# Kernel optimization log

Hardware: AMD Instinct MI355X
Metric: run time of the kernel (lower is better)

Reference implementation:

```python
import jax, jax.numpy as jnp
import numpy as np

B, T, D, H, L, OUT = 16, 48, 256, 8, 3, 6
STYLE, SKILL = 64, 64


def _ln(x, g, b):
    m = jnp.mean(x, -1, keepdims=True)
    v = jnp.mean((x - m) ** 2, -1, keepdims=True)
    return (x - m) * jax.lax.rsqrt(v + 1e-5) * g + b


def _gelu(x):
    return jax.nn.gelu(x, approximate=False)  # torch 'gelu' activation is exact erf form


def _mha(q_in, kv_in, qkv_w, qkv_b, o_w, o_b, mask):
    d = q_in.shape[-1]
    hd = d // H
    wq, wk, wv = jnp.split(qkv_w, 3, 0)
    bq, bk, bv = jnp.split(qkv_b, 3, 0)

    def heads(x, w, b):
        y = x @ w.T + b
        return y.reshape(y.shape[0], y.shape[1], H, hd)

    q, k, v = heads(q_in, wq, bq), heads(kv_in, wk, bk), heads(kv_in, wv, bv)
    s = jnp.einsum('bqhd,bkhd->bhqk', q, k) / np.float32(np.sqrt(hd))
    if mask is not None:
        s = jnp.where(mask, jnp.float32(-1e9), s)
    a = jax.nn.softmax(s, -1)
    o = jnp.einsum('bhqk,bkhd->bqhd', a, v).reshape(q_in.shape[0], q_in.shape[1], d)
    return o @ o_w.T + o_b


def _pos_encoding():
    pos = jnp.arange(T, dtype=jnp.float32)[:, None]
    div = jnp.exp(jnp.arange(0, D, 2, dtype=jnp.float32) * (-np.log(10000.0) / D))
    pe = jnp.zeros((T, D), jnp.float32)
    pe = pe.at[:, 0::2].set(jnp.sin(pos * div))
    pe = pe.at[:, 1::2].set(jnp.cos(pos * div))
    return pe


def setup_inputs() -> dict:
    key = jax.random.key(0)
    ks = iter(jax.random.split(key, 40))

    def rn(shape, s=0.05):
        return jax.random.normal(next(ks), shape, jnp.float32) * s

    return {
        'z_style': jax.random.normal(next(ks), (B, STYLE), jnp.float32),
        'z_skill': jax.random.normal(next(ks), (B, SKILL), jnp.float32),
        'start_token': jnp.zeros((1, 1, OUT), jnp.float32),
        'mem_w1': rn((D, STYLE + SKILL)), 'mem_b1': jnp.zeros((D,), jnp.float32),
        'mem_ln_g': jnp.ones((D,), jnp.float32), 'mem_ln_b': jnp.zeros((D,), jnp.float32),
        'mem_w2': rn((D, D)), 'mem_b2': jnp.zeros((D,), jnp.float32),
        'emb_w': rn((D, OUT)), 'emb_b': jnp.zeros((D,), jnp.float32),
        'sa_qkv_w': rn((L, 3 * D, D)), 'sa_qkv_b': jnp.zeros((L, 3 * D), jnp.float32),
        'sa_o_w': rn((L, D, D)), 'sa_o_b': jnp.zeros((L, D), jnp.float32),
        'ca_qkv_w': rn((L, 3 * D, D)), 'ca_qkv_b': jnp.zeros((L, 3 * D), jnp.float32),
        'ca_o_w': rn((L, D, D)), 'ca_o_b': jnp.zeros((L, D), jnp.float32),
        'ln1_g': jnp.ones((L, D), jnp.float32), 'ln1_b': jnp.zeros((L, D), jnp.float32),
        'ln2_g': jnp.ones((L, D), jnp.float32), 'ln2_b': jnp.zeros((L, D), jnp.float32),
        'ln3_g': jnp.ones((L, D), jnp.float32), 'ln3_b': jnp.zeros((L, D), jnp.float32),
        'ff1_w': rn((L, 4 * D, D)), 'ff1_b': jnp.zeros((L, 4 * D), jnp.float32),
        'ff2_w': rn((L, D, 4 * D)), 'ff2_b': jnp.zeros((L, D), jnp.float32),
        'op_w1': rn((D // 2, D)), 'op_b1': jnp.zeros((D // 2,), jnp.float32),
        'op_w2': rn((OUT, D // 2)), 'op_b2': jnp.zeros((OUT,), jnp.float32),
    }


def reference(z_style, z_skill, start_token, mem_w1, mem_b1, mem_ln_g, mem_ln_b,
              mem_w2, mem_b2, emb_w, emb_b, sa_qkv_w, sa_qkv_b, sa_o_w, sa_o_b,
              ca_qkv_w, ca_qkv_b, ca_o_w, ca_o_b, ln1_g, ln1_b, ln2_g, ln2_b,
              ln3_g, ln3_b, ff1_w, ff1_b, ff2_w, ff2_b, op_w1, op_b1, op_w2, op_b2):
    # memory: [B,1,D] expanded to seq_len (identical rows, as in the torch module)
    cond = jnp.concatenate([z_style, z_skill], -1)
    h = _gelu(_ln(cond @ mem_w1.T + mem_b1, mem_ln_g, mem_ln_b))
    memory = jnp.broadcast_to((h @ mem_w2.T + mem_b2)[:, None, :], (B, T, D))

    pe = _pos_encoding()
    causal = jnp.triu(jnp.ones((T, T), bool), 1)  # True = masked (future)
    layer_ps = (sa_qkv_w, sa_qkv_b, sa_o_w, sa_o_b, ca_qkv_w, ca_qkv_b, ca_o_w,
                ca_o_b, ln1_g, ln1_b, ln2_g, ln2_b, ln3_g, ln3_b,
                ff1_w, ff1_b, ff2_w, ff2_b)

    def layer_step(x, p):
        (sqw, sqb, sow, sob, cqw, cqb, cow, cob, g1, b1, g2, b2, g3, b3,
         f1w, f1b, f2w, f2b) = p
        # post-norm TransformerDecoderLayer (torch default norm_first=False)
        x = _ln(x + _mha(x, x, sqw, sqb, sow, sob, causal), g1, b1)
        x = _ln(x + _mha(x, memory, cqw, cqb, cow, cob, None), g2, b2)
        x = _ln(x + (_gelu(x @ f1w.T + f1b) @ f2w.T + f2b), g3, b3)
        return x, None

    def t_step(inputs, t):
        # Causal mask => decoded[:, t] depends only on inputs[:, :t+1]; running the
        # padded full-length decoder reproduces the torch growing-prefix loop exactly.
        x = inputs @ emb_w.T + emb_b + pe[None]
        dec, _ = jax.lax.scan(layer_step, x, layer_ps)
        d_t = jax.lax.dynamic_slice(dec, (0, t, 0), (B, 1, D))[:, 0]
        out_t = _gelu(d_t @ op_w1.T + op_b1) @ op_w2.T + op_b2
        inputs = jax.lax.dynamic_update_slice(inputs, out_t[:, None, :], (0, t + 1, 0))
        return inputs, out_t

    inputs0 = jnp.zeros((B, T, OUT), jnp.float32).at[:, 0:1, :].set(
        jnp.broadcast_to(start_token, (B, 1, OUT)))
    _, ys = jax.lax.scan(t_step, inputs0, jnp.arange(T))
    return jnp.transpose(ys, (1, 0, 2))  # [B, T, OUT]
```

## Files before the change

kernel.cpp:

```cpp
#include <hip/hip_runtime.h>
#include <hip/hip_bf16.h>
#include <math.h>

#define NGRP 16
#define GWG  8
#define NBLK (NGRP*GWG)
#define NTHR 512
#define TSEQ 48
#define DDIM 256
#define HDIM 32
#define NLAY 3
#define NOUT 6

#define CNT_OFF   0u
#define CNT_BYTES 16384u
#define GRP_OFF   16384u
#define GRP_STRF  5120u
#define PO_F   0
#define PF_F   2048
#define CAL_F  4096
#define WB_OFF 360448u
#define WOFF_QKV 0u
#define WOFF_WO  589824u
#define WOFF_F1  786432u
#define WOFF_F2  1572864u
#define WOFF_OP1 2359296u
#define NCVT     2392064u

typedef __attribute__((address_space(1))) const unsigned int gu32;
typedef __attribute__((address_space(3))) unsigned int lu32;

__device__ __forceinline__ void gl_lds16(const unsigned short* g, unsigned short* l) {
  __builtin_amdgcn_global_load_lds((gu32*)g, (lu32*)l, 16, 0, 0);
}
__device__ __forceinline__ void bfp(unsigned int u, float& lo, float& hi) {
  union { unsigned int i; float f; } a, b;
  a.i = u << 16; b.i = u & 0xffff0000u; lo = a.f; hi = b.f;
}
__device__ __forceinline__ float gelu_exact(float x) {
  return 0.5f * x * (1.0f + erff(x * 0.70710678118654752f));
}
__device__ __forceinline__ float dot8(const uint4& u, const float* x, int k0) {
  float lo, hi, acc = 0.f;
  bfp(u.x, lo, hi); acc += x[k0  ]*lo + x[k0+1]*hi;
  bfp(u.y, lo, hi); acc += x[k0+2]*lo + x[k0+3]*hi;
  bfp(u.z, lo, hi); acc += x[k0+4]*lo + x[k0+5]*hi;
  bfp(u.w, lo, hi); acc += x[k0+6]*lo + x[k0+7]*hi;
  return acc;
}

__global__ void convert_bf16(const float* qkv, const float* ow, const float* f1,
                             const float* f2, const float* w1, unsigned char* ws) {
  __hip_bfloat16* dst = (__hip_bfloat16*)(ws + WB_OFF);
  size_t stride = (size_t)gridDim.x * blockDim.x;
  for (size_t i = (size_t)blockIdx.x * blockDim.x + threadIdx.x; i < NCVT; i += stride) {
    float v;
    if      (i < WOFF_WO)  v = qkv[i];
    else if (i < WOFF_F1)  v = ow[i - WOFF_WO];
    else if (i < WOFF_F2)  v = f1[i - WOFF_F1];
    else if (i < WOFF_OP1) v = f2[i - WOFF_F2];
    else                   v = w1[i - WOFF_OP1];
    dst[i] = __float2bfloat16(v);
  }
}

__global__ void precompute_ca(const float* zs, const float* zk,
                              const float* mw1, const float* mb1,
                              const float* mlg, const float* mlb,
                              const float* mw2, const float* mb2,
                              const float* cqw, const float* cqb,
                              const float* cow, const float* cob,
                              unsigned char* ws) {
  const int g = blockIdx.x & 15, l = blockIdx.x >> 4;
  const int tid = threadIdx.x;
  __shared__ float cond[128], h[256], mvv[256], vv[256], lred[16];

  auto lnstat = [&](float v, float& m, float& rs) {
    float a = v, b = v * v;
    #pragma unroll
    for (int off = 32; off; off >>= 1) { a += __shfl_xor(a, off); b += __shfl_xor(b, off); }
    if ((tid & 63) == 0) { lred[tid >> 6] = a; lred[4 + (tid >> 6)] = b; }
    __syncthreads();
    float sa = lred[0]+lred[1]+lred[2]+lred[3];
    float sb = lred[4]+lred[5]+lred[6]+lred[7];
    m = sa * (1.0f/256.0f);
    rs = rsqrtf(sb * (1.0f/256.0f) - m*m + 1e-5f);
    __syncthreads();
  };

  if (tid < 128) cond[tid] = (tid < 64) ? zs[g*64 + tid] : zk[g*64 + tid - 64];
  __syncthreads();
  float acc = mb1[tid];
  { const float* w = mw1 + (size_t)tid * 128;
    for (int k = 0; k < 128; k += 4) {
      float4 q = *(const float4*)(w + k);
      acc += q.x*cond[k] + q.y*cond[k+1] + q.z*cond[k+2] + q.w*cond[k+3];
    } }
  float m, rs; lnstat(acc, m, rs);
  h[tid] = gelu_exact((acc - m) * rs * mlg[tid] + mlb[tid]);
  __syncthreads();
  float a2 = mb2[tid];
  { const float* w = mw2 + (size_t)tid * 256;
    for (int k = 0; k < 256; k += 4) {
      float4 q = *(const float4*)(w + k);
      a2 += q.x*h[k] + q.y*h[k+1] + q.z*h[k+2] + q.w*h[k+3];
    } }
  mvv[tid] = a2;
  __syncthreads();
  float a3 = cqb[l*768 + 512 + tid];
  { const float* w = cqw + ((size_t)l*768 + 512 + tid) * 256;
    for (int k = 0; k < 256; k += 4) {
      float4 q = *(const float4*)(w + k);
      a3 += q.x*mvv[k] + q.y*mvv[k+1] + q.z*mvv[k+2] + q.w*mvv[k+3];
    } }
  vv[tid] = a3;
  __syncthreads();
  float a4 = cob[l*256 + tid];
  { const float* w = cow + ((size_t)l*256 + tid) * 256;
    for (int k = 0; k < 256; k += 4) {
      float4 q = *(const float4*)(w + k);
      a4 += q.x*vv[k] + q.y*vv[k+1] + q.z*vv[k+2] + q.w*vv[k+3];
    } }
  ((float*)(ws + GRP_OFF))[(size_t)g * GRP_STRF + CAL_F + l*256 + tid] = a4;
}

struct DecP {
  const float *start_token, *emb_w, *emb_b;
  const float *sa_qkv_b, *sa_o_b;
  const float *ln1_g, *ln1_b, *ln2_g, *ln2_b, *ln3_g, *ln3_b;
  const float *ff1_b, *ff2_b;
  const float *op_b1, *op_w2, *op_b2;
  float* out;
  unsigned char* ws;
};

__global__ __launch_bounds__(NTHR, 2) void decoder_persistent(DecP p) {
  const int g = blockIdx.x % NGRP;
  const int s = blockIdx.x / NGRP;
  const int tid = threadIdx.x;

  unsigned int* flg = (unsigned int*)(p.ws + CNT_OFF) + (size_t)g * 256;
  float* grp = (float*)(p.ws + GRP_OFF) + (size_t)g * GRP_STRF;
  float* Po = grp + PO_F;
  float* Pf = grp + PF_F;
  const float* CALW = grp + CAL_F;
  const unsigned short* WB = (const unsigned short*)(p.ws + WB_OFF);

  __shared__ __align__(16) unsigned short Rws[32768];
  __shared__ float xls[DDIM], x2ls[DDIM], red[NTHR], lred[16], fxl[128];
  __shared__ float qb[HDIM], ah[HDIM], sc[64];
  __shared__ float kc[NLAY*TSEQ*33], vc[NLAY*TSEQ*33];
  __shared__ float cals[768], obias[768], ff2b[768];
  __shared__ float ln1g[768], ln1b[768], ln2g[768], ln2b[768], ln3g[768], ln3b[768];
  __shared__ float qkvb[288], ff1b[384];
  __shared__ float embw[DDIM*NOUT], embb[DDIM];
  __shared__ float opb1[128], opw2[NOUT*128], opb2[8], OUTV[8];

  const int olin = tid >> 2, kk = tid & 3;
  const int oB = tid & 255, khB = tid >> 8;
  const int wv = tid >> 6, ln = tid & 63;

  auto stage_qkv = [&](int l) {
    #pragma unroll
    for (int r = 0; r < 6; ++r) {
      int c = (r*8 + wv)*64 + ln;
      int row = c >> 5, wc = (c & 31) ^ (row & 7);
      const unsigned short* gp = WB + WOFF_QKV
        + ((size_t)(l*768 + (row>>5)*256 + s*32 + (row&31)))*256 + wc*8;
      gl_lds16(gp, Rws + (size_t)(r*8 + wv)*512);
    }
  };
  auto stage_ff1 = [&](int l) {
    #pragma unroll
    for (int r = 0; r < 8; ++r) {
      int c = (r*8 + wv)*64 + ln;
      int row = c >> 5, wc = (c & 31) ^ (row & 7);
      const unsigned short* gp = WB + WOFF_F1
        + ((size_t)(l*1024 + s*128 + row))*256 + wc*8;
      gl_lds16(gp, Rws + (size_t)(r*8 + wv)*512);
    }
  };
  auto stage_ff2 = [&](int l) {
    #pragma unroll
    for (int r = 0; r < 8; ++r) {
      int c = (r*8 + wv)*64 + ln;
      int row = c >> 4, wc = (c & 15) ^ (row & 7);
      const unsigned short* gp = WB + WOFF_F2
        + ((size_t)(l*256 + row))*1024 + s*128 + wc*8;
      gl_lds16(gp, Rws + (size_t)(r*8 + wv)*512);
    }
  };

  uint4 pWO[2], pO1[8];
  auto ldWO = [&](int l) {
    const unsigned short* w = WB + WOFF_WO + ((size_t)(l*256 + oB))*256 + s*32 + khB*16;
    pWO[0] = *(const uint4*)(w);
    pWO[1] = *(const uint4*)(w + 8);
  };
  auto ldO1 = [&]() {
    const unsigned short* w = WB + WOFF_OP1 + (size_t)olin*256 + kk*64;
    #pragma unroll
    for (int i = 0; i < 8; ++i) pO1[i] = *(const uint4*)(w + i*8);
  };

  unsigned int barcount = 0;
  auto group_barrier = [&]() {
    __syncthreads();
    ++barcount;
    if (tid == 0)
      __hip_atomic_store(flg + s*32, barcount, __ATOMIC_RELEASE, __HIP_MEMORY_SCOPE_AGENT);
    if (tid < GWG) {
      while (__hip_atomic_load(flg + tid*32, __ATOMIC_RELAXED, __HIP_MEMORY_SCOPE_AGENT) < barcount) {}
    }
    if (tid == 0)
      (void)__hip_atomic_load(flg + s*32, __ATOMIC_ACQUIRE, __HIP_MEMORY_SCOPE_AGENT);
    __syncthreads();
  };

  auto lnstats = [&](float v, float& m, float& rs) {
    float a = v, b = v * v;
    #pragma unroll
    for (int off = 32; off; off >>= 1) { a += __shfl_xor(a, off); b += __shfl_xor(b, off); }
    if ((tid & 63) == 0) { lred[tid >> 6] = a; lred[8 + (tid >> 6)] = b; }
    __syncthreads();
    float sa = lred[0]+lred[1]+lred[2]+lred[3]+lred[4]+lred[5]+lred[6]+lred[7];
    float sb = lred[8]+lred[9]+lred[10]+lred[11]+lred[12]+lred[13]+lred[14]+lred[15];
    m = sa * (1.0f/256.0f);
    rs = rsqrtf(sb * (1.0f/256.0f) - m*m + 1e-5f);
    __syncthreads();
  };

  for (int i = tid; i < 768; i += NTHR) {
    cals[i]  = CALW[i];
    obias[i] = p.sa_o_b[i];
    ff2b[i]  = p.ff2_b[i];
    ln1g[i] = p.ln1_g[i]; ln1b[i] = p.ln1_b[i];
    ln2g[i] = p.ln2_g[i]; ln2b[i] = p.ln2_b[i];
    ln3g[i] = p.ln3_g[i]; ln3b[i] = p.ln3_b[i];
  }
  for (int i = tid; i < 288; i += NTHR) {
    int l = i / 96, r = i % 96, sect = (r >> 5), o = r & 31;
    qkvb[i] = p.sa_qkv_b[l*768 + sect*256 + s*32 + o];
  }
  for (int i = tid; i < 384; i += NTHR) {
    int l = i >> 7, o = i & 127;
    ff1b[i] = p.ff1_b[l*1024 + s*128 + o];
  }
  for (int i = tid; i < DDIM*NOUT; i += NTHR) embw[i] = p.emb_w[i];
  for (int i = tid; i < DDIM; i += NTHR) embb[i] = p.emb_b[i];
  for (int i = tid; i < 128; i += NTHR) opb1[i] = p.op_b1[i];
  for (int i = tid; i < NOUT*128; i += NTHR) opw2[i] = p.op_w2[i];
  if (tid < NOUT) { opb2[tid] = p.op_b2[tid]; OUTV[tid] = p.start_token[tid]; }

  const float divv = (tid < 256) ? expf(-0.035977892078031968f * (float)(2*(tid>>1))) : 0.f;

  stage_qkv(0);
  ldWO(0);
  __syncthreads();

  for (int t = 0; t < TSEQ; ++t) {
    for (int l = 0; l < NLAY; ++l) {
      if (l == 0) {
        __syncthreads();
        if (tid < 256) {
          float ang = (float)t * divv;
          float pe = (tid & 1) ? cosf(ang) : sinf(ang);
          float acc = embb[tid] + pe;
          #pragma unroll
          for (int j = 0; j < NOUT; ++j) acc += OUTV[j] * embw[tid*NOUT + j];
          xls[tid] = acc;
        }
      } else {
        float r2 = 0.f;
        if (tid < 256) {
          r2 = x2ls[tid] + ff2b[(l-1)*256 + tid];
          #pragma unroll
          for (int ss = 0; ss < GWG; ++ss) r2 += Pf[ss*256 + tid];
        }
        float m, rs; lnstats(r2, m, rs);
        if (tid < 256)
          xls[tid] = (r2 - m) * rs * ln3g[(l-1)*256 + tid] + ln3b[(l-1)*256 + tid];
      }
      __syncthreads();
      if (olin < 96) {
        float acc = 0.f;
        #pragma unroll
        for (int i = 0; i < 8; ++i) {
          int ii = (i + kk) & 7;
          int k0 = kk*64 + ii*8;
          const uint4 w = *(const uint4*)(Rws + olin*256 + (k0 ^ ((olin&7)<<3)));
          acc += dot8(w, xls, k0);
        }
        red[tid] = acc;
      }
      __syncthreads();
      stage_ff1(l);
      if (tid < 96) {
        float v = red[tid*4] + red[tid*4+1] + red[tid*4+2] + red[tid*4+3] + qkvb[l*96 + tid];
        int sect = tid >> 5, o = tid & 31;
        if (sect == 0) qb[o] = v;
        else if (sect == 1) kc[(l*TSEQ + t)*33 + o] = v;
        else vc[(l*TSEQ + t)*33 + o] = v;
      }
      __syncthreads();
      if (tid < 64) {
        float scj = -1e30f;
        if (tid <= t) {
          const float* kr = &kc[(l*TSEQ + tid)*33];
          float a = 0.f;
          #pragma unroll
          for (int d = 0; d < HDIM; ++d) a += qb[d] * kr[d];
          scj = a * 0.17677669529663687f;
        }
        float mx = scj;
        #pragma unroll
        for (int off = 32; off; off >>= 1) mx = fmaxf(mx, __shfl_xor(mx, off));
        float e = (tid <= t) ? expf(scj - mx) : 0.f;
        float su = e;
        #pragma unroll
        for (int off = 32; off; off >>= 1) su += __shfl_xor(su, off);
        sc[tid] = e / su;
      }
      __syncthreads();
      if (tid < 256) {
        int d = tid >> 3, jg = tid & 7;
        float acc = 0.f;
        for (int j = jg; j <= t; j += 8) acc += sc[j] * vc[(l*TSEQ + j)*33 + d];
        acc += __shfl_xor(acc, 1);
        acc += __shfl_xor(acc, 2);
        acc += __shfl_xor(acc, 4);
        if (jg == 0) ah[d] = acc;
      }
      __syncthreads();
      red[tid] = dot8(pWO[0], ah, khB*16) + dot8(pWO[1], ah, khB*16 + 8);
      __syncthreads();
      if (tid < 256) Po[s*256 + tid] = red[tid] + red[tid + 256];
      group_barrier();

      float r = 0.f;
      if (tid < 256) {
        r = xls[tid] + obias[l*256 + tid];
        #pragma unroll
        for (int ss = 0; ss < GWG; ++ss) r += Po[ss*256 + tid];
      }
      float m1, rs1; lnstats(r, m1, rs1);
      float z = 0.f;
      if (tid < 256)
        z = (r - m1)*rs1*ln1g[l*256 + tid] + ln1b[l*256 + tid] + cals[l*256 + tid];
      float m2, rs2; lnstats(z, m2, rs2);
      if (tid < 256) x2ls[tid] = (z - m2)*rs2*ln2g[l*256 + tid] + ln2b[l*256 + tid];
      __syncthreads();
      {
        float acc = 0.f;
        #pragma unroll
        for (int i = 0; i < 8; ++i) {
          int ii = (i + kk) & 7;
          int k0 = kk*64 + ii*8;
          const uint4 w = *(const uint4*)(Rws + olin*256 + (k0 ^ ((olin&7)<<3)));
          acc += dot8(w, x2ls, k0);
        }
        red[tid] = acc;
      }
      __syncthreads();
      stage_ff2(l);
      if (tid < 128)
        fxl[tid] = gelu_exact(red[tid*4] + red[tid*4+1] + red[tid*4+2] + red[tid*4+3]
                              + ff1b[l*128 + tid]);
      __syncthreads();
      {
        float acc = 0.f;
        #pragma unroll
        for (int j = 0; j < 8; ++j) {
          int k0 = khB*64 + j*8;
          const uint4 w = *(const uint4*)(Rws + oB*128 + (k0 ^ ((oB&7)<<3)));
          acc += dot8(w, fxl, k0);
        }
        red[tid] = acc;
      }
      __syncthreads();
      {
        int lnx = (l == 2) ? 0 : l + 1;
        stage_qkv(lnx);
        ldWO(lnx);
        if (l == 2) ldO1();
      }
      if (tid < 256) Pf[s*256 + tid] = red[tid] + red[tid + 256];
      group_barrier();
    }

    {
      float r2 = 0.f;
      if (tid < 256) {
        r2 = x2ls[tid] + ff2b[2*256 + tid];
        #pragma unroll
        for (int ss = 0; ss < GWG; ++ss) r2 += Pf[ss*256 + tid];
      }
      float m, rs; lnstats(r2, m, rs);
      if (tid < 256) xls[tid] = (r2 - m)*rs*ln3g[2*256 + tid] + ln3b[2*256 + tid];
      __syncthreads();
      float oacc = 0.f;
      #pragma unroll
      for (int i = 0; i < 8; ++i) oacc += dot8(pO1[i], xls, kk*64 + i*8);
      red[tid] = oacc;
      __syncthreads();
      if (tid < 128)
        fxl[tid] = gelu_exact(red[tid*4] + red[tid*4+1] + red[tid*4+2] + red[tid*4+3]
                              + opb1[tid]);
      __syncthreads();
      if (tid < 192) {
        int oo = tid >> 5, kl = tid & 31;
        float acc = fxl[kl]*opw2[oo*128 + kl] + fxl[kl+32]*opw2[oo*128 + kl+32]
                  + fxl[kl+64]*opw2[oo*128 + kl+64] + fxl[kl+96]*opw2[oo*128 + kl+96];
        #pragma unroll
        for (int off = 16; off; off >>= 1) acc += __shfl_xor(acc, off);
        if (kl == 0) {
          float v = acc + opb2[oo];
          OUTV[oo] = v;
          if (s == 0) p.out[((size_t)g*TSEQ + t)*NOUT + oo] = v;
        }
      }
    }
  }
}

extern "C" void kernel_launch(void* const* d_in, const int* in_sizes, int n_in,
                              void* d_out, int out_size, void* d_ws, size_t ws_size,
                              hipStream_t stream) {
  const float* const* F = (const float* const*)d_in;
  const float* z_style = F[0]; const float* z_skill = F[1];
  DecP p;
  p.start_token = F[2];
  const float* mem_w1 = F[3]; const float* mem_b1 = F[4];
  const float* mem_ln_g = F[5]; const float* mem_ln_b = F[6];
  const float* mem_w2 = F[7]; const float* mem_b2 = F[8];
  p.emb_w = F[9]; p.emb_b = F[10];
  const float* sa_qkv_w = F[11]; p.sa_qkv_b = F[12];
  const float* sa_o_w  = F[13]; p.sa_o_b = F[14];
  const float* ca_qkv_w = F[15]; const float* ca_qkv_b = F[16];
  const float* ca_o_w = F[17]; const float* ca_o_b = F[18];
  p.ln1_g = F[19]; p.ln1_b = F[20]; p.ln2_g = F[21]; p.ln2_b = F[22];
  p.ln3_g = F[23]; p.ln3_b = F[24];
  const float* ff1_w = F[25]; p.ff1_b = F[26];
  const float* ff2_w = F[27]; p.ff2_b = F[28];
  const float* op_w1 = F[29]; p.op_b1 = F[30]; p.op_w2 = F[31]; p.op_b2 = F[32];
  p.out = (float*)d_out;
  p.ws  = (unsigned char*)d_ws;

  hipMemsetAsync((char*)d_ws + CNT_OFF, 0, CNT_BYTES, stream);
  convert_bf16<<<dim3(512), dim3(256), 0, stream>>>(sa_qkv_w, sa_o_w, ff1_w, ff2_w, op_w1,
                                                    (unsigned char*)d_ws);
  precompute_ca<<<dim3(48), dim3(256), 0, stream>>>(z_style, z_skill, mem_w1, mem_b1,
                                                    mem_ln_g, mem_ln_b, mem_w2, mem_b2,
                                                    ca_qkv_w, ca_qkv_b, ca_o_w, ca_o_b,
                                                    (unsigned char*)d_ws);
  decoder_persistent<<<dim3(NBLK), dim3(NTHR), 0, stream>>>(p);
}
```

Baseline: 2.202 ms.

## Cut block barriers with shuffle reductions and overlap weight staging with group barrier

Replaces the shared-memory red[] reduction plus extra __syncthreads with quad shuffle reductions in the QKV, FF1 and output-projection GEMVs. Attention scores and the AV product are fused so each wave handles its own slice. The output projection and FF2 now use one thread per output row with no cross-half reduction. LayerNorm stats use separate slots so the trailing barrier can be dropped, and the next stage's weight staging is issued inside the cross-block group barrier wait. The embedding for the next step is computed at the end of the previous step, and launch bounds change to one block per SM. The aim is to shorten the serial per-token critical path, at the cost of some idle threads and a changed FF2 swizzle that must match the reads.

```diff
diff --git a/kernel.cpp b/kernel.cpp
--- a/kernel.cpp
+++ b/kernel.cpp
@@ -134,7 +134,7 @@
   unsigned char* ws;
 };
 
-__global__ __launch_bounds__(NTHR, 2) void decoder_persistent(DecP p) {
+__global__ __launch_bounds__(NTHR, 1) void decoder_persistent(DecP p) {
   const int g = blockIdx.x % NGRP;
   const int s = blockIdx.x / NGRP;
   const int tid = threadIdx.x;
@@ -147,8 +147,8 @@
   const unsigned short* WB = (const unsigned short*)(p.ws + WB_OFF);
 
   __shared__ __align__(16) unsigned short Rws[32768];
-  __shared__ float xls[DDIM], x2ls[DDIM], red[NTHR], lred[16], fxl[128];
-  __shared__ float qb[HDIM], ah[HDIM], sc[64];
+  __shared__ float xls[DDIM], x2ls[DDIM], lred[32], fxl[128];
+  __shared__ float qb[HDIM], ah[HDIM], scw[8*64];
   __shared__ float kc[NLAY*TSEQ*33], vc[NLAY*TSEQ*33];
   __shared__ float cals[768], obias[768], ff2b[768];
   __shared__ float ln1g[768], ln1b[768], ln2g[768], ln2b[768], ln3g[768], ln3b[768];
@@ -156,17 +156,16 @@
   __shared__ float embw[DDIM*NOUT], embb[DDIM];
   __shared__ float opb1[128], opw2[NOUT*128], opb2[8], OUTV[8];
 
-  const int olin = tid >> 2, kk = tid & 3;
-  const int oB = tid & 255, khB = tid >> 8;
+  const int row = tid >> 2, kk = tid & 3;
   const int wv = tid >> 6, ln = tid & 63;
 
   auto stage_qkv = [&](int l) {
     #pragma unroll
     for (int r = 0; r < 6; ++r) {
       int c = (r*8 + wv)*64 + ln;
-      int row = c >> 5, wc = (c & 31) ^ (row & 7);
+      int rw = c >> 5, wc = (c & 31) ^ (rw & 7);
       const unsigned short* gp = WB + WOFF_QKV
-        + ((size_t)(l*768 + (row>>5)*256 + s*32 + (row&31)))*256 + wc*8;
+        + ((size_t)(l*768 + (rw>>5)*256 + s*32 + (rw&31)))*256 + wc*8;
       gl_lds16(gp, Rws + (size_t)(r*8 + wv)*512);
     }
   };
@@ -174,9 +173,9 @@
     #pragma unroll
     for (int r = 0; r < 8; ++r) {
       int c = (r*8 + wv)*64 + ln;
-      int row = c >> 5, wc = (c & 31) ^ (row & 7);
+      int rw = c >> 5, wc = (c & 31) ^ (rw & 7);
       const unsigned short* gp = WB + WOFF_F1
-        + ((size_t)(l*1024 + s*128 + row))*256 + wc*8;
+        + ((size_t)(l*1024 + s*128 + rw))*256 + wc*8;
       gl_lds16(gp, Rws + (size_t)(r*8 + wv)*512);
     }
   };
@@ -184,31 +183,34 @@
     #pragma unroll
     for (int r = 0; r < 8; ++r) {
       int c = (r*8 + wv)*64 + ln;
-      int row = c >> 4, wc = (c & 15) ^ (row & 7);
+      int rw = c >> 4, wc = (c & 15) ^ (rw & 15);
       const unsigned short* gp = WB + WOFF_F2
-        + ((size_t)(l*256 + row))*1024 + s*128 + wc*8;
+        + ((size_t)(l*256 + rw))*1024 + s*128 + wc*8;
       gl_lds16(gp, Rws + (size_t)(r*8 + wv)*512);
     }
   };
 
-  uint4 pWO[2], pO1[8];
+  uint4 pWO[4], pO1[8];
   auto ldWO = [&](int l) {
-    const unsigned short* w = WB + WOFF_WO + ((size_t)(l*256 + oB))*256 + s*32 + khB*16;
-    pWO[0] = *(const uint4*)(w);
-    pWO[1] = *(const uint4*)(w + 8);
+    if (tid < 256) {
+      const unsigned short* w = WB + WOFF_WO + ((size_t)(l*256 + tid))*256 + s*32;
+      #pragma unroll
+      for (int c = 0; c < 4; ++c) pWO[c] = *(const uint4*)(w + c*8);
+    }
   };
   auto ldO1 = [&]() {
-    const unsigned short* w = WB + WOFF_OP1 + (size_t)olin*256 + kk*64;
+    const unsigned short* w = WB + WOFF_OP1 + (size_t)row*256 + kk*64;
     #pragma unroll
     for (int i = 0; i < 8; ++i) pO1[i] = *(const uint4*)(w + i*8);
   };
 
   unsigned int barcount = 0;
-  auto group_barrier = [&]() {
+  auto gbar = [&](auto stager) {
     __syncthreads();
     ++barcount;
     if (tid == 0)
       __hip_atomic_store(flg + s*32, barcount, __ATOMIC_RELEASE, __HIP_MEMORY_SCOPE_AGENT);
+    stager();
     if (tid < GWG) {
       while (__hip_atomic_load(flg + tid*32, __ATOMIC_RELAXED, __HIP_MEMORY_SCOPE_AGENT) < barcount) {}
     }
@@ -217,17 +219,16 @@
     __syncthreads();
   };
 
-  auto lnstats = [&](float v, float& m, float& rs) {
+  auto lnstats = [&](float v, float* slot, float& m, float& rs) {
     float a = v, b = v * v;
     #pragma unroll
     for (int off = 32; off; off >>= 1) { a += __shfl_xor(a, off); b += __shfl_xor(b, off); }
-    if ((tid & 63) == 0) { lred[tid >> 6] = a; lred[8 + (tid >> 6)] = b; }
+    if ((tid & 63) == 0 && tid < 256) { slot[tid >> 6] = a; slot[4 + (tid >> 6)] = b; }
     __syncthreads();
-    float sa = lred[0]+lred[1]+lred[2]+lred[3]+lred[4]+lred[5]+lred[6]+lred[7];
-    float sb = lred[8]+lred[9]+lred[10]+lred[11]+lred[12]+lred[13]+lred[14]+lred[15];
+    float sa = slot[0]+slot[1]+slot[2]+slot[3];
+    float sb = slot[4]+slot[5]+slot[6]+slot[7];
     m = sa * (1.0f/256.0f);
     rs = rsqrtf(sb * (1.0f/256.0f) - m*m + 1e-5f);
-    __syncthreads();
   };
 
   for (int i = tid; i < 768; i += NTHR) {
@@ -250,63 +251,61 @@
   for (int i = tid; i < DDIM; i += NTHR) embb[i] = p.emb_b[i];
   for (int i = tid; i < 128; i += NTHR) opb1[i] = p.op_b1[i];
   for (int i = tid; i < NOUT*128; i += NTHR) opw2[i] = p.op_w2[i];
-  if (tid < NOUT) { opb2[tid] = p.op_b2[tid]; OUTV[tid] = p.start_token[tid]; }
+  if (tid < NOUT) OUTV[tid] = p.start_token[tid];
+  if (tid < 8) opb2[tid] = (tid < NOUT) ? p.op_b2[tid] : 0.f;
 
   const float divv = (tid < 256) ? expf(-0.035977892078031968f * (float)(2*(tid>>1))) : 0.f;
-
+  __syncthreads();
+
+  if (tid < 256) {
+    float acc = embb[tid] + ((tid & 1) ? 1.0f : 0.0f);
+    #pragma unroll
+    for (int j = 0; j < NOUT; ++j) acc += OUTV[j] * embw[tid*NOUT + j];
+    xls[tid] = acc;
+  }
   stage_qkv(0);
   ldWO(0);
   __syncthreads();
 
   for (int t = 0; t < TSEQ; ++t) {
     for (int l = 0; l < NLAY; ++l) {
-      if (l == 0) {
-        __syncthreads();
-        if (tid < 256) {
-          float ang = (float)t * divv;
-          float pe = (tid & 1) ? cosf(ang) : sinf(ang);
-          float acc = embb[tid] + pe;
-          #pragma unroll
-          for (int j = 0; j < NOUT; ++j) acc += OUTV[j] * embw[tid*NOUT + j];
-          xls[tid] = acc;
-        }
-      } else {
+      if (l > 0) {
         float r2 = 0.f;
         if (tid < 256) {
           r2 = x2ls[tid] + ff2b[(l-1)*256 + tid];
           #pragma unroll
           for (int ss = 0; ss < GWG; ++ss) r2 += Pf[ss*256 + tid];
         }
-        float m, rs; lnstats(r2, m, rs);
+        float m, rs; lnstats(r2, lred + 0, m, rs);
         if (tid < 256)
           xls[tid] = (r2 - m) * rs * ln3g[(l-1)*256 + tid] + ln3b[(l-1)*256 + tid];
-      }
-      __syncthreads();
-      if (olin < 96) {
+        __syncthreads();
+      }
+      if (row < 96) {
         float acc = 0.f;
         #pragma unroll
         for (int i = 0; i < 8; ++i) {
           int ii = (i + kk) & 7;
           int k0 = kk*64 + ii*8;
-          const uint4 w = *(const uint4*)(Rws + olin*256 + (k0 ^ ((olin&7)<<3)));
+          const uint4 w = *(const uint4*)(Rws + row*256 + (k0 ^ ((row&7)<<3)));
           acc += dot8(w, xls, k0);
         }
-        red[tid] = acc;
-      }
-      __syncthreads();
-      stage_ff1(l);
-      if (tid < 96) {
-        float v = red[tid*4] + red[tid*4+1] + red[tid*4+2] + red[tid*4+3] + qkvb[l*96 + tid];
-        int sect = tid >> 5, o = tid & 31;
-        if (sect == 0) qb[o] = v;
-        else if (sect == 1) kc[(l*TSEQ + t)*33 + o] = v;
-        else vc[(l*TSEQ + t)*33 + o] = v;
-      }
-      __syncthreads();
-      if (tid < 64) {
+        acc += __shfl_xor(acc, 1);
+        acc += __shfl_xor(acc, 2);
+        if (kk == 0) {
+          float v = acc + qkvb[l*96 + row];
+          int sect = row >> 5, o = row & 31;
+          if (sect == 0) qb[o] = v;
+          else if (sect == 1) kc[(l*TSEQ + t)*33 + o] = v;
+          else vc[(l*TSEQ + t)*33 + o] = v;
+        }
+      }
+      __syncthreads();
+      {
+        int j = ln;
         float scj = -1e30f;
-        if (tid <= t) {
-          const float* kr = &kc[(l*TSEQ + tid)*33];
+        if (j <= t) {
+          const float* kr = &kc[(l*TSEQ + j)*33];
           float a = 0.f;
           #pragma unroll
           for (int d = 0; d < HDIM; ++d) a += qb[d] * kr[d];
@@ -315,27 +314,29 @@
         float mx = scj;
         #pragma unroll
         for (int off = 32; off; off >>= 1) mx = fmaxf(mx, __shfl_xor(mx, off));
-        float e = (tid <= t) ? expf(scj - mx) : 0.f;
+        float e = (j <= t) ? expf(scj - mx) : 0.f;
         float su = e;
         #pragma unroll
         for (int off = 32; off; off >>= 1) su += __shfl_xor(su, off);
-        sc[tid] = e / su;
+        scw[wv*64 + j] = e / su;
+        int jg = ln >> 2, dd = ln & 3, d = wv*4 + dd;
+        float acc = 0.f;
+        for (int jj = jg; jj <= t; jj += 16)
+          acc += scw[wv*64 + jj] * vc[(l*TSEQ + jj)*33 + d];
+        acc += __shfl_xor(acc, 4);
+        acc += __shfl_xor(acc, 8);
+        acc += __shfl_xor(acc, 16);
+        acc += __shfl_xor(acc, 32);
+        if (ln < 4) ah[wv*4 + ln] = acc;
       }
       __syncthreads();
       if (tid < 256) {
-        int d = tid >> 3, jg = tid & 7;
         float acc = 0.f;
-        for (int j = jg; j <= t; j += 8) acc += sc[j] * vc[(l*TSEQ + j)*33 + d];
-        acc += __shfl_xor(acc, 1);
-        acc += __shfl_xor(acc, 2);
-        acc += __shfl_xor(acc, 4);
-        if (jg == 0) ah[d] = acc;
-      }
-      __syncthreads();
-      red[tid] = dot8(pWO[0], ah, khB*16) + dot8(pWO[1], ah, khB*16 + 8);
-      __syncthreads();
-      if (tid < 256) Po[s*256 + tid] = red[tid] + red[tid + 256];
-      group_barrier();
+        #pragma unroll
+        for (int c = 0; c < 4; ++c) acc += dot8(pWO[c], ah, c*8);
+        Po[s*256 + tid] = acc;
+      }
+      gbar([&]{ stage_ff1(l); });
 
       float r = 0.f;
       if (tid < 256) {
@@ -343,49 +344,45 @@
         #pragma unroll
         for (int ss = 0; ss < GWG; ++ss) r += Po[ss*256 + tid];
       }
-      float m1, rs1; lnstats(r, m1, rs1);
+      float m1, rs1; lnstats(r, lred + 8, m1, rs1);
       float z = 0.f;
       if (tid < 256)
         z = (r - m1)*rs1*ln1g[l*256 + tid] + ln1b[l*256 + tid] + cals[l*256 + tid];
-      float m2, rs2; lnstats(z, m2, rs2);
+      float m2, rs2; lnstats(z, lred + 16, m2, rs2);
       if (tid < 256) x2ls[tid] = (z - m2)*rs2*ln2g[l*256 + tid] + ln2b[l*256 + tid];
       __syncthreads();
+      float facc = 0.f;
       {
-        float acc = 0.f;
         #pragma unroll
         for (int i = 0; i < 8; ++i) {
           int ii = (i + kk) & 7;
           int k0 = kk*64 + ii*8;
-          const uint4 w = *(const uint4*)(Rws + olin*256 + (k0 ^ ((olin&7)<<3)));
-          acc += dot8(w, x2ls, k0);
-        }
-        red[tid] = acc;
+          const uint4 w = *(const uint4*)(Rws + row*256 + (k0 ^ ((row&7)<<3)));
+          facc += dot8(w, x2ls, k0);
+        }
+        facc += __shfl_xor(facc, 1);
+        facc += __shfl_xor(facc, 2);
       }
       __syncthreads();
       stage_ff2(l);
-      if (tid < 128)
-        fxl[tid] = gelu_exact(red[tid*4] + red[tid*4+1] + red[tid*4+2] + red[tid*4+3]
-                              + ff1b[l*128 + tid]);
-      __syncthreads();
-      {
-        float acc = 0.f;
-        #pragma unroll
-        for (int j = 0; j < 8; ++j) {
-          int k0 = khB*64 + j*8;
-          const uint4 w = *(const uint4*)(Rws + oB*128 + (k0 ^ ((oB&7)<<3)));
-          acc += dot8(w, fxl, k0);
-        }
-        red[tid] = acc;
-      }
-      __syncthreads();
+      if (kk == 0) fxl[row] = gelu_exact(facc + ff1b[l*128 + row]);
+      __syncthreads();
+      if (tid < 256) {
+        float acc2 = 0.f;
+        #pragma unroll
+        for (int j2 = 0; j2 < 16; ++j2) {
+          int k0 = j2*8;
+          const uint4 w = *(const uint4*)(Rws + tid*128 + (k0 ^ ((tid&15)<<3)));
+          acc2 += dot8(w, fxl, k0);
+        }
+        Pf[s*256 + tid] = acc2;
+      }
       {
         int lnx = (l == 2) ? 0 : l + 1;
-        stage_qkv(lnx);
         ldWO(lnx);
         if (l == 2) ldO1();
       }
-      if (tid < 256) Pf[s*256 + tid] = red[tid] + red[tid + 256];
-      group_barrier();
+      gbar([&]{ stage_qkv((l == 2) ? 0 : l + 1); });
     }
 
     {
@@ -395,17 +392,15 @@
         #pragma unroll
         for (int ss = 0; ss < GWG; ++ss) r2 += Pf[ss*256 + tid];
       }
-      float m, rs; lnstats(r2, m, rs);
+      float m, rs; lnstats(r2, lred + 24, m, rs);
       if (tid < 256) xls[tid] = (r2 - m)*rs*ln3g[2*256 + tid] + ln3b[2*256 + tid];
       __syncthreads();
       float oacc = 0.f;
       #pragma unroll
       for (int i = 0; i < 8; ++i) oacc += dot8(pO1[i], xls, kk*64 + i*8);
-      red[tid] = oacc;
-      __syncthreads();
-      if (tid < 128)
-        fxl[tid] = gelu_exact(red[tid*4] + red[tid*4+1] + red[tid*4+2] + red[tid*4+3]
-                              + opb1[tid]);
+      oacc += __shfl_xor(oacc, 1);
+      oacc += __shfl_xor(oacc, 2);
+      if (kk == 0) fxl[row] = gelu_exact(oacc + opb1[row]);
       __syncthreads();
       if (tid < 192) {
         int oo = tid >> 5, kl = tid & 31;
@@ -419,6 +414,16 @@
           if (s == 0) p.out[((size_t)g*TSEQ + t)*NOUT + oo] = v;
         }
       }
+      __syncthreads();
+      if (tid < 256) {
+        float ang = (float)(t + 1) * divv;
+        float pe = (tid & 1) ? cosf(ang) : sinf(ang);
+        float acc = embb[tid] + pe;
+        #pragma unroll
+        for (int j = 0; j < NOUT; ++j) acc += OUTV[j] * embw[tid*NOUT + j];
+        xls[tid] = acc;
+      }
+      __syncthreads();
     }
   }
 }
```

Result: slower. 2.712 ms (+23.2%).
